# Kernel optimization log

Hardware: AMD Instinct MI355X
Metric: run time of the kernel (lower is better)

The kernel has to match this reference:

```python
import jax, jax.numpy as jnp
import numpy as np

H = 16          # num_attention_heads
D_MODEL = 1024  # hidden_size
D_HEAD = D_MODEL // H


def setup_inputs() -> dict:
    key = jax.random.key(0)
    ks = jax.random.split(key, 8)
    B, S = 4, 2048
    s = 1.0 / np.sqrt(D_MODEL)
    return {
        "hidden_states": jax.random.normal(ks[0], (B, S, D_MODEL), jnp.float32),
        "attention_mask": jnp.zeros((B, 1, 1, S), jnp.float32),
        "Wq": jax.random.normal(ks[1], (D_MODEL, D_MODEL), jnp.float32) * s,
        "bq": jnp.zeros((D_MODEL,), jnp.float32),
        "Wk": jax.random.normal(ks[2], (D_MODEL, D_MODEL), jnp.float32) * s,
        "bk": jnp.zeros((D_MODEL,), jnp.float32),
        "Wv": jax.random.normal(ks[3], (D_MODEL, D_MODEL), jnp.float32) * s,
        "bv": jnp.zeros((D_MODEL,), jnp.float32),
    }


def reference(hidden_states, attention_mask, Wq, bq, Wk, bk, Wv, bv):
    B, S, _ = hidden_states.shape
    # QKV projections, split into heads: [B, H, S, d]
    def proj(W, b):
        x = hidden_states @ W + b
        return x.reshape(B, S, H, D_HEAD).transpose(0, 2, 1, 3)

    q = proj(Wq, bq)
    k = proj(Wk, bk)
    v = proj(Wv, bv)

    scores = jnp.einsum('bhqd,bhkd->bhqk', q, k) / np.sqrt(D_HEAD)
    scores = scores + attention_mask
    probs = jax.nn.softmax(scores, axis=-1)  # dropout prob = 0 (eval)
    ctx = jnp.einsum('bhqk,bhkd->bhqd', probs, v)
    return ctx.transpose(0, 2, 1, 3).reshape(B, S, D_MODEL)
```

## Files before the change

kernel.cpp:

```cpp
#include <hip/hip_runtime.h>
#include <hip/hip_bf16.h>


typedef float  f32x4  __attribute__((ext_vector_type(4)));
typedef float  f32x16 __attribute__((ext_vector_type(16)));
typedef short  short8 __attribute__((ext_vector_type(8)));
typedef __bf16 bf16x8 __attribute__((ext_vector_type(8)));
typedef unsigned int uint4v __attribute__((ext_vector_type(4)));

#define AS1 __attribute__((address_space(1)))
#define AS3 __attribute__((address_space(3)))

__device__ __forceinline__ void gload_lds16(const void* g, void* l) {
    __builtin_amdgcn_global_load_lds((const AS1 void*)g, (AS3 void*)l, 16, 0, 0);
}

__device__ __forceinline__ unsigned short f2bf(float f) {
    union { float f; unsigned int u; } v; v.f = f;
    unsigned int u = v.u;
    unsigned int r = (u + 0x7fffu + ((u >> 16) & 1u)) >> 16;
    return (unsigned short)r;
}

__device__ __forceinline__ unsigned packbf(float a, float b) {
    unsigned short lo = __builtin_bit_cast(unsigned short, (__bf16)a);
    unsigned short hh = __builtin_bit_cast(unsigned short, (__bf16)b);
    return (unsigned)lo | ((unsigned)hh << 16);
}

__device__ __forceinline__ f32x4 mfma16(short8 a, short8 b, f32x4 c) {
    return __builtin_amdgcn_mfma_f32_16x16x32_bf16(
        __builtin_bit_cast(bf16x8, a), __builtin_bit_cast(bf16x8, b), c, 0, 0, 0);
}

__device__ __forceinline__ f32x16 mfma32(short8 a, short8 b, f32x16 c) {
    return __builtin_amdgcn_mfma_f32_32x32x16_bf16(
        __builtin_bit_cast(bf16x8, a), __builtin_bit_cast(bf16x8, b), c, 0, 0, 0);
}

__device__ __forceinline__ f32x16 mfma32u(uint4v a, short8 b, f32x16 c) {
    return __builtin_amdgcn_mfma_f32_32x32x16_bf16(
        __builtin_bit_cast(bf16x8, a), __builtin_bit_cast(bf16x8, b), c, 0, 0, 0);
}


__global__ void conv_x(const float* __restrict__ X, unsigned short* __restrict__ Xb, int n4) {
    int i = blockIdx.x * blockDim.x + threadIdx.x;
    int stride = gridDim.x * blockDim.x;
    for (; i < n4; i += stride) {
        float4 v = ((const float4*)X)[i];
        ushort4 o;
        o.x = f2bf(v.x); o.y = f2bf(v.y); o.z = f2bf(v.z); o.w = f2bf(v.w);
        ((ushort4*)Xb)[i] = o;
    }
}

__global__ void conv_w_t(const float* __restrict__ Wq, const float* __restrict__ Wk,
                         const float* __restrict__ Wv,
                         unsigned short* __restrict__ Wqt, unsigned short* __restrict__ Wkt,
                         unsigned short* __restrict__ Wvt) {
    const float* W = (blockIdx.z == 0) ? Wq : (blockIdx.z == 1) ? Wk : Wv;
    unsigned short* Wt = (blockIdx.z == 0) ? Wqt : (blockIdx.z == 1) ? Wkt : Wvt;
    __shared__ unsigned short tile[64][65];
    int n0 = blockIdx.x * 64, k0 = blockIdx.y * 64;
    int t = threadIdx.x;
    int cr = t >> 6, cc = t & 63;
    for (int i = 0; i < 16; i++) {
        int row = i * 4 + cr;
        tile[row][cc] = f2bf(W[(size_t)(k0 + row) * 1024 + n0 + cc]);
    }
    __syncthreads();
    for (int i = 0; i < 16; i++) {
        int row = i * 4 + cr;
        Wt[(size_t)(n0 + row) * 1024 + k0 + cc] = tile[cc][row];
    }
}


__global__ __launch_bounds__(256)
void gemm_qk(const unsigned short* __restrict__ A,
             const unsigned short* __restrict__ Bt0, const unsigned short* __restrict__ Bt1,
             const float* __restrict__ bias0, const float* __restrict__ bias1,
             unsigned short* __restrict__ o0, unsigned short* __restrict__ o1) {
    __shared__ unsigned short Alds[2][4096];
    __shared__ unsigned short Blds[2][4096];
    const int K = 1024;
    const int z = blockIdx.z;
    const unsigned short* Bt = z ? Bt1 : Bt0;
    const float* bias = z ? bias1 : bias0;
    unsigned short* out = z ? o1 : o0;
    const float scale = z ? 1.0f : 0.125f;

    int t = threadIdx.x;
    int m0 = blockIdx.y * 128, n0 = blockIdx.x * 128;
    int wid = t >> 6, lane = t & 63, g = lane >> 4, r16 = lane & 15;
    int wr = wid >> 1, wc = wid & 1;

    f32x4 acc[4][4] = {};

    const unsigned short* Ab = A + (size_t)(m0 + (t >> 2)) * K + (t & 3) * 8;
    const unsigned short* Bb = Bt + (size_t)(n0 + (t >> 2)) * K + (t & 3) * 8;

#define STAGE_G(buf, k0)                                              \
    gload_lds16(Ab + (k0), &Alds[buf][wid * 512]);                    \
    gload_lds16(Ab + (k0) + (size_t)64 * K, &Alds[buf][2048 + wid * 512]); \
    gload_lds16(Bb + (k0), &Blds[buf][wid * 512]);                    \
    gload_lds16(Bb + (k0) + (size_t)64 * K, &Blds[buf][2048 + wid * 512]);

    STAGE_G(0, 0)
    asm volatile("s_waitcnt vmcnt(0)" ::: "memory");
    __syncthreads();

    int cur = 0;
    for (int k0 = 0; k0 < K; k0 += 32) {
        if (k0 + 32 < K) { STAGE_G(cur ^ 1, k0 + 32) }
        short8 af[4], bfr[4];
        #pragma unroll
        for (int m = 0; m < 4; m++)
            af[m] = *(const short8*)&Alds[cur][(wr * 64 + m * 16 + r16) * 32 + g * 8];
        #pragma unroll
        for (int n = 0; n < 4; n++)
            bfr[n] = *(const short8*)&Blds[cur][(wc * 64 + n * 16 + r16) * 32 + g * 8];
        #pragma unroll
        for (int m = 0; m < 4; m++)
            #pragma unroll
            for (int n = 0; n < 4; n++)
                acc[m][n] = mfma16(af[m], bfr[n], acc[m][n]);
        asm volatile("s_waitcnt vmcnt(0)" ::: "memory");
        __syncthreads();
        cur ^= 1;
    }

    for (int m = 0; m < 4; m++) {
        int gmBase = m0 + wr * 64 + m * 16 + g * 4;
        for (int n = 0; n < 4; n++) {
            int gn = n0 + wc * 64 + n * 16 + r16;
            float bcol = bias[gn];
            for (int r = 0; r < 4; r++) {
                int gm = gmBase + r;
                float v = (acc[m][n][r] + bcol) * scale;
                int b = gm >> 11, s = gm & 2047, h = gn >> 6, d = gn & 63;
                out[((size_t)(b * 16 + h) * 2048 + s) * 64 + d] = f2bf(v);
            }
        }
    }
}


__global__ __launch_bounds__(256)
void gemm_v(const unsigned short* __restrict__ A, const unsigned short* __restrict__ Bt,
            const float* __restrict__ bias, unsigned short* __restrict__ out) {
    __shared__ unsigned short Alds[2][4096];
    __shared__ unsigned short Blds[2][4096];
    const int K = 1024, N = 8192;

    int t = threadIdx.x;
    int m0 = blockIdx.y * 128, n0 = blockIdx.x * 128;
    int wid = t >> 6, lane = t & 63, g = lane >> 4, r16 = lane & 15;
    int wr = wid >> 1, wc = wid & 1;

    f32x4 acc[4][4] = {};

    const unsigned short* Ab = A + (size_t)(m0 + (t >> 2)) * K + (t & 3) * 8;
    const unsigned short* Bb = Bt + (size_t)(n0 + (t >> 2)) * K + (t & 3) * 8;

    STAGE_G(0, 0)
    asm volatile("s_waitcnt vmcnt(0)" ::: "memory");
    __syncthreads();

    int cur = 0;
    for (int k0 = 0; k0 < K; k0 += 32) {
        if (k0 + 32 < K) { STAGE_G(cur ^ 1, k0 + 32) }
        short8 af[4], bfr[4];
        #pragma unroll
        for (int m = 0; m < 4; m++)
            af[m] = *(const short8*)&Alds[cur][(wr * 64 + m * 16 + r16) * 32 + g * 8];
        #pragma unroll
        for (int n = 0; n < 4; n++)
            bfr[n] = *(const short8*)&Blds[cur][(wc * 64 + n * 16 + r16) * 32 + g * 8];
        #pragma unroll
        for (int m = 0; m < 4; m++)
            #pragma unroll
            for (int n = 0; n < 4; n++)
                acc[m][n] = mfma16(af[m], bfr[n], acc[m][n]);
        asm volatile("s_waitcnt vmcnt(0)" ::: "memory");
        __syncthreads();
        cur ^= 1;
    }

    for (int m = 0; m < 4; m++) {
        int gmBase = m0 + wr * 64 + m * 16 + g * 4;
        for (int n = 0; n < 4; n++) {
            int gn = n0 + wc * 64 + n * 16 + r16;
            for (int r = 0; r < 4; r++) {
                int gm = gmBase + r;
                out[(size_t)gm * N + gn] = f2bf(acc[m][n][r] + bias[gm]);
            }
        }
    }
}


__global__ __launch_bounds__(256, 2)
void attn(const unsigned short* __restrict__ Qb, const unsigned short* __restrict__ Kb,
          const unsigned short* __restrict__ Vtb, const float* __restrict__ mask,
          float* __restrict__ out) {
    __shared__ unsigned short Kl[2][8192];
    __shared__ unsigned short Vl[2][8192];
    __shared__ float sums[4][64];

    const int t = threadIdx.x, wid = t >> 6, lane = t & 63;
    const int hi = lane >> 5, c = lane & 31;
    const int bh = blockIdx.x, b = bh >> 4, h = bh & 15;
    const int q0w = blockIdx.y * 256 + wid * 64;

    short8 qf[2][4];
    #pragma unroll
    for (int qh = 0; qh < 2; qh++)
        #pragma unroll
        for (int ds = 0; ds < 4; ds++)
            qf[qh][ds] = *(const short8*)&Qb[((size_t)bh * 2048 + q0w + qh * 32 + c) * 64
                                             + ds * 16 + hi * 8];

    float lsum[2] = {0.f, 0.f};
    f32x16 ctx[2][2] = {};

    const int srow = t >> 3;
    const int schk = (t & 7) ^ (srow & 7);
    const unsigned short* Kst = Kb + (size_t)bh * 2048 * 64 + srow * 64 + schk * 8;
    const int vd = t >> 4;
    const int vchk = (t & 15) ^ (vd & 7);
    const unsigned short* Vst = Vtb + (size_t)(h * 64 + vd) * 8192 + (size_t)b * 2048 + vchk * 8;
    const float* mrow = mask + (size_t)b * 2048;

#define STAGE_KV(buf, T0)                                                         \
    gload_lds16(Kst + (size_t)(T0) * 64,         &Kl[buf][wid * 512]);            \
    gload_lds16(Kst + (size_t)((T0) + 32) * 64,  &Kl[buf][2048 + wid * 512]);     \
    gload_lds16(Kst + (size_t)((T0) + 64) * 64,  &Kl[buf][4096 + wid * 512]);     \
    gload_lds16(Kst + (size_t)((T0) + 96) * 64,  &Kl[buf][6144 + wid * 512]);     \
    gload_lds16(Vst + (T0),                      &Vl[buf][wid * 512]);            \
    gload_lds16(Vst + (T0) + (size_t)16 * 8192,  &Vl[buf][2048 + wid * 512]);     \
    gload_lds16(Vst + (T0) + (size_t)32 * 8192,  &Vl[buf][4096 + wid * 512]);     \
    gload_lds16(Vst + (T0) + (size_t)48 * 8192,  &Vl[buf][6144 + wid * 512]);

    STAGE_KV(0, 0)
    asm volatile("s_waitcnt vmcnt(0)" ::: "memory");
    __syncthreads();

    int cur = 0;
    for (int t0 = 0; t0 < 2048; t0 += 128) {
        if (t0 + 128 < 2048) { STAGE_KV(cur ^ 1, t0 + 128) }
        const unsigned short* K_ = Kl[cur];
        const unsigned short* V_ = Vl[cur];

        #pragma unroll
        for (int kb = 0; kb < 4; kb++) {
            const int krow = kb * 32 + c;
            short8 kf[4];
            #pragma unroll
            for (int ds = 0; ds < 4; ds++)
                kf[ds] = *(const short8*)&K_[krow * 64 + (((ds * 2 + hi) ^ (krow & 7)) * 8)];
            float4 m4[4];
            #pragma unroll
            for (int q = 0; q < 4; q++)
                m4[q] = *(const float4*)&mrow[t0 + kb * 32 + q * 8 + hi * 4];

            uint4v pa[2][2];
            #pragma unroll
            for (int qh = 0; qh < 2; qh++) {
                f32x16 st;
                #pragma unroll
                for (int q = 0; q < 4; q++) {
                    st[q * 4 + 0] = m4[q].x; st[q * 4 + 1] = m4[q].y;
                    st[q * 4 + 2] = m4[q].z; st[q * 4 + 3] = m4[q].w;
                }
                __builtin_amdgcn_s_setprio(1);
                #pragma unroll
                for (int ds = 0; ds < 4; ds++)
                    st = mfma32(kf[ds], qf[qh][ds], st);
                __builtin_amdgcn_s_setprio(0);
                float p[16];
                #pragma unroll
                for (int r = 0; r < 16; r++) {
                    p[r] = __expf(st[r]);
                    lsum[qh] += p[r];
                }
                unsigned cc[8];
                #pragma unroll
                for (int i = 0; i < 8; i++) cc[i] = packbf(p[2 * i], p[2 * i + 1]);
                unsigned w[8];
                #pragma unroll
                for (int i = 0; i < 2; i++) {
                    {
                        unsigned u = hi ? cc[i] : cc[i + 2];
                        unsigned s = __shfl_xor(u, 32);
                        w[i]     = hi ? s : cc[i];
                        w[i + 2] = hi ? cc[i + 2] : s;
                    }
                    {
                        unsigned u = hi ? cc[i + 4] : cc[i + 6];
                        unsigned s = __shfl_xor(u, 32);
                        w[i + 4] = hi ? s : cc[i + 4];
                        w[i + 6] = hi ? cc[i + 6] : s;
                    }
                }
                pa[qh][0] = (uint4v){w[0], w[1], w[2], w[3]};
                pa[qh][1] = (uint4v){w[4], w[5], w[6], w[7]};
            }

            __builtin_amdgcn_s_setprio(1);
            #pragma unroll
            for (int db = 0; db < 2; db++) {
                const int vrow = db * 32 + c;
                #pragma unroll
                for (int tl = 0; tl < 2; tl++) {
                    const int chunk = (kb * 2 + tl) * 2 + hi;
                    short8 vf = *(const short8*)&V_[vrow * 128 + ((chunk ^ (vrow & 7)) * 8)];
                    ctx[0][db] = mfma32u(pa[0][tl], vf, ctx[0][db]);
                    ctx[1][db] = mfma32u(pa[1][tl], vf, ctx[1][db]);
                }
            }
            __builtin_amdgcn_s_setprio(0);
        }

        asm volatile("s_waitcnt vmcnt(0)" ::: "memory");
        __syncthreads();
        cur ^= 1;
    }

    #pragma unroll
    for (int qh = 0; qh < 2; qh++) {
        float tot = lsum[qh] + __shfl_xor(lsum[qh], 32);
        if (hi == 0) sums[wid][qh * 32 + c] = tot;
    }
    __syncthreads();
    #pragma unroll
    for (int qh = 0; qh < 2; qh++) {
        #pragma unroll
        for (int rg = 0; rg < 4; rg++) {
            float4 sv = *(const float4*)&sums[wid][qh * 32 + rg * 8 + hi * 4];
            float svf[4] = {sv.x, sv.y, sv.z, sv.w};
            #pragma unroll
            for (int r = 0; r < 4; r++) {
                const float inv = 1.f / svf[r];
                const int reg = rg * 4 + r;
                const int row = q0w + qh * 32 + rg * 8 + hi * 4 + r;
                out[((size_t)b * 2048 + row) * 1024 + h * 64 + c]      = ctx[qh][0][reg] * inv;
                out[((size_t)b * 2048 + row) * 1024 + h * 64 + 32 + c] = ctx[qh][1][reg] * inv;
            }
        }
    }
}


extern "C" void kernel_launch(void* const* d_in, const int* in_sizes, int n_in,
                              void* d_out, int out_size, void* d_ws, size_t ws_size,
                              hipStream_t stream) {
    const float* X    = (const float*)d_in[0];
    const float* mask = (const float*)d_in[1];
    const float* Wq   = (const float*)d_in[2];
    const float* bq   = (const float*)d_in[3];
    const float* Wk   = (const float*)d_in[4];
    const float* bk   = (const float*)d_in[5];
    const float* Wv   = (const float*)d_in[6];
    const float* bv   = (const float*)d_in[7];
    float* out = (float*)d_out;

    unsigned short* ws  = (unsigned short*)d_ws;
    unsigned short* Xb  = ws;
    unsigned short* Wqt = Xb + 8388608;
    unsigned short* Wkt = Wqt + 1048576;
    unsigned short* Wvt = Wkt + 1048576;
    unsigned short* Qb  = Wvt + 1048576;
    unsigned short* Kb  = Qb + 8388608;
    unsigned short* Vtb = Kb + 8388608;

    conv_x<<<2048, 256, 0, stream>>>(X, Xb, 2097152);
    conv_w_t<<<dim3(16, 16, 3), 256, 0, stream>>>(Wq, Wk, Wv, Wqt, Wkt, Wvt);

    gemm_qk<<<dim3(8, 64, 2), 256, 0, stream>>>(Xb, Wqt, Wkt, bq, bk, Qb, Kb);
    gemm_v<<<dim3(64, 8), 256, 0, stream>>>(Wvt, Xb, bv, Vtb);

    attn<<<dim3(64, 8), 256, 0, stream>>>(Qb, Kb, Vtb, mask, out);
}
```

Before: 279.9 us.

## Use exp2 softmax with prescaled Q/mask and halve attention block and key tile

Folds log2(e) into the Q projection scale and a pre-scaled mask so the softmax uses the native exp2 instruction instead of __expf. Shrinks the attention kernel to 128-thread blocks covering 128 queries, with 64-key double-buffered K/V tiles, and doubles the grid. This is meant to raise occupancy and lower LDS per block and per-exp cost. The trade-off is more loop iterations and barriers, plus more redundant K/V global loads per query.

```diff
diff --git a/kernel.cpp b/kernel.cpp
--- a/kernel.cpp
+++ b/kernel.cpp
@@ -76,6 +76,11 @@
     }
 }
 
+__global__ void conv_mask(const float* __restrict__ m, float* __restrict__ o, int n) {
+    int i = blockIdx.x * blockDim.x + threadIdx.x;
+    if (i < n) o[i] = m[i] * 1.4426950408889634f;
+}
+
 
 __global__ __launch_bounds__(256)
 void gemm_qk(const unsigned short* __restrict__ A,
@@ -89,7 +94,7 @@
     const unsigned short* Bt = z ? Bt1 : Bt0;
     const float* bias = z ? bias1 : bias0;
     unsigned short* out = z ? o1 : o0;
-    const float scale = z ? 1.0f : 0.125f;
+    const float scale = z ? 1.0f : 0.18033688011112042f;
 
     int t = threadIdx.x;
     int m0 = blockIdx.y * 128, n0 = blockIdx.x * 128;
@@ -201,18 +206,18 @@
 }
 
 
-__global__ __launch_bounds__(256, 2)
+__global__ __launch_bounds__(128, 2)
 void attn(const unsigned short* __restrict__ Qb, const unsigned short* __restrict__ Kb,
-          const unsigned short* __restrict__ Vtb, const float* __restrict__ mask,
+          const unsigned short* __restrict__ Vtb, const float* __restrict__ msc,
           float* __restrict__ out) {
-    __shared__ unsigned short Kl[2][8192];
-    __shared__ unsigned short Vl[2][8192];
-    __shared__ float sums[4][64];
+    __shared__ unsigned short Kl[2][4096];
+    __shared__ unsigned short Vl[2][4096];
+    __shared__ float sums[2][64];
 
     const int t = threadIdx.x, wid = t >> 6, lane = t & 63;
     const int hi = lane >> 5, c = lane & 31;
     const int bh = blockIdx.x, b = bh >> 4, h = bh & 15;
-    const int q0w = blockIdx.y * 256 + wid * 64;
+    const int q0w = blockIdx.y * 128 + wid * 64;
 
     short8 qf[2][4];
     #pragma unroll
@@ -225,36 +230,32 @@
     float lsum[2] = {0.f, 0.f};
     f32x16 ctx[2][2] = {};
 
-    const int srow = t >> 3;
-    const int schk = (t & 7) ^ (srow & 7);
-    const unsigned short* Kst = Kb + (size_t)bh * 2048 * 64 + srow * 64 + schk * 8;
-    const int vd = t >> 4;
-    const int vchk = (t & 15) ^ (vd & 7);
-    const unsigned short* Vst = Vtb + (size_t)(h * 64 + vd) * 8192 + (size_t)b * 2048 + vchk * 8;
-    const float* mrow = mask + (size_t)b * 2048;
-
-#define STAGE_KV(buf, T0)                                                         \
-    gload_lds16(Kst + (size_t)(T0) * 64,         &Kl[buf][wid * 512]);            \
-    gload_lds16(Kst + (size_t)((T0) + 32) * 64,  &Kl[buf][2048 + wid * 512]);     \
-    gload_lds16(Kst + (size_t)((T0) + 64) * 64,  &Kl[buf][4096 + wid * 512]);     \
-    gload_lds16(Kst + (size_t)((T0) + 96) * 64,  &Kl[buf][6144 + wid * 512]);     \
-    gload_lds16(Vst + (T0),                      &Vl[buf][wid * 512]);            \
-    gload_lds16(Vst + (T0) + (size_t)16 * 8192,  &Vl[buf][2048 + wid * 512]);     \
-    gload_lds16(Vst + (T0) + (size_t)32 * 8192,  &Vl[buf][4096 + wid * 512]);     \
-    gload_lds16(Vst + (T0) + (size_t)48 * 8192,  &Vl[buf][6144 + wid * 512]);
+    const int l3 = lane >> 3;
+    const int sRow = wid * 8 + l3;
+    const int sChk = (lane & 7) ^ (l3 & 7);
+    const unsigned short* Kst = Kb + (size_t)bh * 2048 * 64 + sRow * 64 + sChk * 8;
+    const unsigned short* Vst = Vtb + (size_t)(h * 64 + sRow) * 8192 + (size_t)b * 2048 + sChk * 8;
+    const float* mrow = msc + (size_t)b * 2048;
+
+#define STAGE_KV(buf, T0)                                                             \
+    _Pragma("unroll")                                                                 \
+    for (int i = 0; i < 4; i++) {                                                     \
+        gload_lds16(Kst + (size_t)(T0) * 64 + i * 1024, &Kl[buf][wid * 512 + i * 1024]); \
+        gload_lds16(Vst + (T0) + (size_t)i * 16 * 8192, &Vl[buf][wid * 512 + i * 1024]); \
+    }
 
     STAGE_KV(0, 0)
     asm volatile("s_waitcnt vmcnt(0)" ::: "memory");
     __syncthreads();
 
     int cur = 0;
-    for (int t0 = 0; t0 < 2048; t0 += 128) {
-        if (t0 + 128 < 2048) { STAGE_KV(cur ^ 1, t0 + 128) }
+    for (int t0 = 0; t0 < 2048; t0 += 64) {
+        if (t0 + 64 < 2048) { STAGE_KV(cur ^ 1, t0 + 64) }
         const unsigned short* K_ = Kl[cur];
         const unsigned short* V_ = Vl[cur];
 
         #pragma unroll
-        for (int kb = 0; kb < 4; kb++) {
+        for (int kb = 0; kb < 2; kb++) {
             const int krow = kb * 32 + c;
             short8 kf[4];
             #pragma unroll
@@ -282,7 +283,7 @@
                 float p[16];
                 #pragma unroll
                 for (int r = 0; r < 16; r++) {
-                    p[r] = __expf(st[r]);
+                    p[r] = __builtin_amdgcn_exp2f(st[r]);
                     lsum[qh] += p[r];
                 }
                 unsigned cc[8];
@@ -315,7 +316,7 @@
                 #pragma unroll
                 for (int tl = 0; tl < 2; tl++) {
                     const int chunk = (kb * 2 + tl) * 2 + hi;
-                    short8 vf = *(const short8*)&V_[vrow * 128 + ((chunk ^ (vrow & 7)) * 8)];
+                    short8 vf = *(const short8*)&V_[vrow * 64 + ((chunk ^ (vrow & 7)) * 8)];
                     ctx[0][db] = mfma32u(pa[0][tl], vf, ctx[0][db]);
                     ctx[1][db] = mfma32u(pa[1][tl], vf, ctx[1][db]);
                 }
@@ -374,12 +375,14 @@
     unsigned short* Qb  = Wvt + 1048576;
     unsigned short* Kb  = Qb + 8388608;
     unsigned short* Vtb = Kb + 8388608;
+    float* msc = (float*)(Vtb + 8388608);
 
     conv_x<<<2048, 256, 0, stream>>>(X, Xb, 2097152);
     conv_w_t<<<dim3(16, 16, 3), 256, 0, stream>>>(Wq, Wk, Wv, Wqt, Wkt, Wvt);
+    conv_mask<<<32, 256, 0, stream>>>(mask, msc, 8192);
 
     gemm_qk<<<dim3(8, 64, 2), 256, 0, stream>>>(Xb, Wqt, Wkt, bq, bk, Qb, Kb);
     gemm_v<<<dim3(64, 8), 256, 0, stream>>>(Wvt, Xb, bv, Vtb);
 
-    attn<<<dim3(64, 8), 256, 0, stream>>>(Qb, Kb, Vtb, mask, out);
-}
+    attn<<<dim3(64, 16), 128, 0, stream>>>(Qb, Kb, Vtb, msc, out);
+}
```

New measurement: 290.4 us. 1.04x slower.
